# Kernel optimization log

Measured on AMD Instinct MI355X. Metric: run time of the kernel, lower is better.

Reference implementation:

```python
import jax, jax.numpy as jnp
import numpy as np


def _add_self_loops(edge_index, num_nodes):
    loops = jnp.arange(num_nodes, dtype=edge_index.dtype)
    row = jnp.concatenate([edge_index[0], loops])
    col = jnp.concatenate([edge_index[1], loops])
    return row, col


def _gcn_norm(row, col, num_nodes):
    # deg computed at aggregation targets (col), edge weights all 1 (PyG gcn_norm)
    deg = jax.ops.segment_sum(jnp.ones_like(col, dtype=jnp.float32), col,
                              num_segments=num_nodes)
    dinv = jnp.where(deg > 0, jax.lax.rsqrt(deg), 0.0)
    return dinv[row] * dinv[col]  # [E+N]


def _gcn_conv(x, row, col, norm, W, b, num_nodes):
    h = x @ W                                  # [N, out] linear first (PyG GCNConv)
    msg = h[row] * norm[:, None]               # gather + scale, [E+N, out]
    agg = jax.ops.segment_sum(msg, col, num_segments=num_nodes)
    return agg + b


def setup_inputs() -> dict:
    key = jax.random.key(0)
    N, F, H, E = 100000, 128, 64, 1600000
    k1, k2, k3, k4 = jax.random.split(key, 4)
    x = jax.random.normal(k1, (N, F), dtype=jnp.float32)
    edge_index = jax.random.randint(k2, (2, E), 0, N, dtype=jnp.int64)
    s1 = 1.0 / np.sqrt(F)
    s2 = 1.0 / np.sqrt(H)
    W1 = jax.random.normal(k3, (F, H), dtype=jnp.float32) * s1
    b1 = jnp.zeros((H,), dtype=jnp.float32)
    W2 = jax.random.normal(k4, (H, 1), dtype=jnp.float32) * s2
    b2 = jnp.zeros((1,), dtype=jnp.float32)
    return {"x": x, "edge_index": edge_index, "W1": W1, "b1": b1,
            "W2": W2, "b2": b2}


def reference(x, edge_index, W1, b1, W2, b2):
    N = x.shape[0]
    row, col = _add_self_loops(edge_index, N)
    norm = _gcn_norm(row, col, N)
    h = jax.nn.relu(_gcn_conv(x, row, col, norm, W1, b1, N))
    # dropout p=0.0 -> identity
    out = _gcn_conv(h, row, col, norm, W2, b2, N)
    return out.reshape(-1)  # [N]
```

## Files before the change

### kernel.cpp

```cpp
#include <hip/hip_runtime.h>
#include <hip/hip_bf16.h>


#define SHIFT 9
#define BMASK ((1 << SHIFT) - 1)

__device__ __forceinline__ bool detect_i64(const unsigned* u) {
    unsigned acc = 0;
#pragma unroll
    for (int i = 1; i <= 32; ++i) acc |= u[2 * i + 1];
    return acc == 0u;
}

__device__ __forceinline__ int load_edge(const void* ei, bool is64, long long idx) {
    if (is64) return ((const int*)ei)[idx << 1];
    return ((const int*)ei)[idx];
}

__device__ __forceinline__ unsigned bf16_rn(float x) {
    unsigned u = __float_as_uint(x);
    return (u + 0x7fffu + ((u >> 16) & 1u)) >> 16;
}
__device__ __forceinline__ unsigned pack_bf2(float a, float b) {
    return bf16_rn(a) | (bf16_rn(b) << 16);
}
__device__ __forceinline__ float bflo(unsigned v) { return __uint_as_float(v << 16); }
__device__ __forceinline__ float bfhi(unsigned v) {
    return __uint_as_float(v & 0xffff0000u);
}

__global__ __launch_bounds__(256) void binA_kernel(const void* ei, int* gcursor,
                                                   unsigned* __restrict__ pairs, int E,
                                                   int cap) {
    bool is64 = detect_i64((const unsigned*)ei);
    __shared__ int whist[4][256];
    __shared__ int bcur[256];
    int t = threadIdx.x;
    int wid = t >> 6;
    long long per = ((long long)E + gridDim.x - 1) / gridDim.x;
    long long e0 = (long long)blockIdx.x * per;
    long long e1 = e0 + per;
    if (e1 > E) e1 = E;
    whist[0][t] = 0; whist[1][t] = 0; whist[2][t] = 0; whist[3][t] = 0;
    __syncthreads();
    for (long long e = e0 + t; e < e1; e += 256) {
        int c = load_edge(ei, is64, (long long)E + e);
        atomicAdd(&whist[wid][c >> SHIFT], 1);
    }
    __syncthreads();
    int tot = whist[0][t] + whist[1][t] + whist[2][t] + whist[3][t];
    int rel = tot ? atomicAdd(&gcursor[t], tot) : 0;
    bcur[t] = t * cap + rel;
    __syncthreads();
    for (long long e = e0 + t; e < e1; e += 256) {
        int r = load_edge(ei, is64, e);
        int c = load_edge(ei, is64, (long long)E + e);
        int b = c >> SHIFT;
        int rk = atomicAdd(&bcur[b], 1);
        pairs[rk] = ((unsigned)r << SHIFT) | (unsigned)(c & BMASK);
    }
}

__global__ __launch_bounds__(256) void binB_kernel(const unsigned* __restrict__ pairs,
                                                   const int* __restrict__ gcursor,
                                                   int* __restrict__ csr,
                                                   int* __restrict__ offs,
                                                   int* __restrict__ deg, int N,
                                                   int cap) {
    __shared__ int cnt[1 << SHIFT];
    __shared__ int cur[1 << SHIFT];
    __shared__ int tmp[256];
    int b = blockIdx.x, t = threadIdx.x;
    int start = b * cap, end = b * cap + gcursor[b];
    cnt[t] = 0;
    cnt[t + 256] = 0;
    __syncthreads();
    for (int i = start + t; i < end; i += 256) atomicAdd(&cnt[pairs[i] & BMASK], 1);
    __syncthreads();
    int c0 = cnt[2 * t], c1 = cnt[2 * t + 1];
    int s = c0 + c1;
    tmp[t] = s;
    __syncthreads();
    for (int off = 1; off < 256; off <<= 1) {
        int xv = (t >= off) ? tmp[t - off] : 0;
        __syncthreads();
        tmp[t] += xv;
        __syncthreads();
    }
    int excl = tmp[t] - s;
    int p0 = start + excl;
    int p1 = p0 + c0;
    cur[2 * t] = p0;
    cur[2 * t + 1] = p1;
    int node0 = (b << SHIFT) + 2 * t;
    if (node0 < N) { offs[node0] = p0; deg[node0] = c0; }
    if (node0 + 1 < N) { offs[node0 + 1] = p1; deg[node0 + 1] = c1; }
    __syncthreads();
    for (int i = start + t; i < end; i += 256) {
        unsigned p = pairs[i];
        int pos = atomicAdd(&cur[p & BMASK], 1);
        csr[pos] = (int)(p >> SHIFT);
    }
}

__device__ __forceinline__ void fma4(float4& a, float s, const float4& w) {
    a.x = fmaf(s, w.x, a.x);
    a.y = fmaf(s, w.y, a.y);
    a.z = fmaf(s, w.z, a.z);
    a.w = fmaf(s, w.w, a.w);
}

__global__ __launch_bounds__(256) void gemm1_kernel(const float* __restrict__ x,
                                                    const float* __restrict__ W1,
                                                    const int* __restrict__ deg,
                                                    unsigned* __restrict__ hs_u, int N) {
    __shared__ float xs[64][132];
    __shared__ float Wl[128][64];
    int t = threadIdx.x;
    const float4* W4 = (const float4*)W1;
    float4* Wl4 = (float4*)&Wl[0][0];
#pragma unroll
    for (int i = 0; i < 8; ++i) Wl4[t + 256 * i] = W4[t + 256 * i];
    int row0 = blockIdx.x * 64;
    const float4* x4 = (const float4*)x;
#pragma unroll
    for (int i = 0; i < 8; ++i) {
        int idx = t + 256 * i;
        int r = idx >> 5;
        int gr = row0 + r;
        float4 v = (gr < N) ? x4[(long long)gr * 32 + (idx & 31)]
                            : make_float4(0.f, 0.f, 0.f, 0.f);
        *(float4*)&xs[r][(idx & 31) * 4] = v;
    }
    __syncthreads();
    int rg = t >> 4;
    int cg = t & 15;
    float4 acc[4];
#pragma unroll
    for (int i = 0; i < 4; ++i) acc[i] = make_float4(0.f, 0.f, 0.f, 0.f);
#pragma unroll 2
    for (int kk = 0; kk < 128; kk += 4) {
        float4 w0 = *(const float4*)&Wl[kk + 0][cg * 4];
        float4 w1 = *(const float4*)&Wl[kk + 1][cg * 4];
        float4 w2 = *(const float4*)&Wl[kk + 2][cg * 4];
        float4 w3 = *(const float4*)&Wl[kk + 3][cg * 4];
#pragma unroll
        for (int i = 0; i < 4; ++i) {
            float4 xv = *(const float4*)&xs[rg * 4 + i][kk];
            fma4(acc[i], xv.x, w0);
            fma4(acc[i], xv.y, w1);
            fma4(acc[i], xv.z, w2);
            fma4(acc[i], xv.w, w3);
        }
    }
#pragma unroll
    for (int i = 0; i < 4; ++i) {
        int gr = row0 + rg * 4 + i;
        if (gr < N) {
            float dinv = rsqrtf((float)deg[gr] + 1.0f);
            unsigned u0 = pack_bf2(acc[i].x * dinv, acc[i].y * dinv);
            unsigned u1 = pack_bf2(acc[i].z * dinv, acc[i].w * dinv);
            *(uint2*)&hs_u[(size_t)gr * 32 + cg * 2] = make_uint2(u0, u1);
        }
    }
}

#define ACC8(v)                                    \
    a0 += bflo((v).x); a1 += bfhi((v).x);          \
    a2 += bflo((v).y); a3 += bfhi((v).y);          \
    a4 += bflo((v).z); a5 += bfhi((v).z);          \
    a6 += bflo((v).w); a7 += bfhi((v).w);

#define RED8(off)                                  \
    a0 += __shfl_xor(a0, off); a1 += __shfl_xor(a1, off); \
    a2 += __shfl_xor(a2, off); a3 += __shfl_xor(a3, off); \
    a4 += __shfl_xor(a4, off); a5 += __shfl_xor(a5, off); \
    a6 += __shfl_xor(a6, off); a7 += __shfl_xor(a7, off);

__global__ __launch_bounds__(256) void pull1_kernel(
    const uint4* __restrict__ hs4, const int* __restrict__ offs,
    const int* __restrict__ deg, const int* __restrict__ csr,
    const float* __restrict__ b1, const float* __restrict__ W2,
    float* __restrict__ hs2, int N) {
    int gid = blockIdx.x * blockDim.x + threadIdx.x;
    int w = gid >> 6;
    if (w >= N) return;
    int lane = gid & 63;
    int oid = lane >> 3;
    int k = lane & 7;
    int s = offs[w];
    int cnt = deg[w];
    float dinv = rsqrtf((float)cnt + 1.0f);
    float a0 = 0.f, a1 = 0.f, a2 = 0.f, a3 = 0.f;
    float a4 = 0.f, a5 = 0.f, a6 = 0.f, a7 = 0.f;
    if (oid == 0) {
        uint4 v = hs4[(size_t)w * 8 + k];
        ACC8(v);
    }
    for (int base = 0; base < cnt; base += 64) {
        int rem = cnt - base;
        int m = rem < 64 ? rem : 64;
        int r = (lane < m) ? csr[s + base + lane] : 0;
        int tt = 0;
        for (; tt + 32 <= m; tt += 32) {
            int r0 = __shfl(r, tt + oid);
            int r1 = __shfl(r, tt + 8 + oid);
            int r2 = __shfl(r, tt + 16 + oid);
            int r3 = __shfl(r, tt + 24 + oid);
            uint4 v0 = hs4[(size_t)r0 * 8 + k];
            uint4 v1 = hs4[(size_t)r1 * 8 + k];
            uint4 v2 = hs4[(size_t)r2 * 8 + k];
            uint4 v3 = hs4[(size_t)r3 * 8 + k];
            ACC8(v0); ACC8(v1); ACC8(v2); ACC8(v3);
        }
        for (; tt + 8 <= m; tt += 8) {
            int rr = __shfl(r, tt + oid);
            uint4 v = hs4[(size_t)rr * 8 + k];
            ACC8(v);
        }
        if (tt < m) {
            int idx = tt + oid;
            int rr = __shfl(r, idx < m ? idx : 0);
            if (idx < m) {
                uint4 v = hs4[(size_t)rr * 8 + k];
                ACC8(v);
            }
        }
    }
    RED8(8); RED8(16); RED8(32);
    float4 bA = ((const float4*)b1)[2 * k];
    float4 bB = ((const float4*)b1)[2 * k + 1];
    float4 wA = ((const float4*)W2)[2 * k];
    float4 wB = ((const float4*)W2)[2 * k + 1];
    float p = fmaxf(fmaf(dinv, a0, bA.x), 0.f) * wA.x
            + fmaxf(fmaf(dinv, a1, bA.y), 0.f) * wA.y
            + fmaxf(fmaf(dinv, a2, bA.z), 0.f) * wA.z
            + fmaxf(fmaf(dinv, a3, bA.w), 0.f) * wA.w
            + fmaxf(fmaf(dinv, a4, bB.x), 0.f) * wB.x
            + fmaxf(fmaf(dinv, a5, bB.y), 0.f) * wB.y
            + fmaxf(fmaf(dinv, a6, bB.z), 0.f) * wB.z
            + fmaxf(fmaf(dinv, a7, bB.w), 0.f) * wB.w;
    p += __shfl_xor(p, 1);
    p += __shfl_xor(p, 2);
    p += __shfl_xor(p, 4);
    if (lane == 0) hs2[w] = dinv * p;
}

__global__ __launch_bounds__(256) void pull2_kernel(
    const float* __restrict__ hs2, const int* __restrict__ offs,
    const int* __restrict__ deg, const int* __restrict__ csr,
    const float* __restrict__ b2, float* __restrict__ out, int N) {
    int i = blockIdx.x * blockDim.x + threadIdx.x;
    if (i >= N) return;
    int s = offs[i];
    int cnt = deg[i];
    float dinv = rsqrtf((float)cnt + 1.0f);
    float a0 = hs2[i];
    float a1 = 0.f, a2 = 0.f, a3 = 0.f;
    int kk = 0;
    for (; kk + 4 <= cnt; kk += 4) {
        a0 += hs2[csr[s + kk]];
        a1 += hs2[csr[s + kk + 1]];
        a2 += hs2[csr[s + kk + 2]];
        a3 += hs2[csr[s + kk + 3]];
    }
    for (; kk < cnt; ++kk) a0 += hs2[csr[s + kk]];
    out[i] = fmaf(dinv, (a0 + a1) + (a2 + a3), b2[0]);
}

extern "C" void kernel_launch(void* const* d_in, const int* in_sizes, int n_in,
                              void* d_out, int out_size, void* d_ws, size_t ws_size,
                              hipStream_t stream) {
    const float* x = (const float*)d_in[0];
    const void* ei = d_in[1];
    const float* W1 = (const float*)d_in[2];
    const float* b1 = (const float*)d_in[3];
    const float* W2 = (const float*)d_in[4];
    const float* b2 = (const float*)d_in[5];
    float* out = (float*)d_out;

    int N = in_sizes[0] / 128;
    int E = in_sizes[1] / 2;
    int NB = (N + (1 << SHIFT) - 1) >> SHIFT;
    int cap = ((2 * (E / NB)) / 256 + 2) * 256;

    char* p = (char*)d_ws;
    unsigned* hs_u = (unsigned*)p;  p += (size_t)N * 32 * sizeof(unsigned);
    float* hs2 = (float*)p;         p += (size_t)N * sizeof(float);
    int* offs = (int*)p;            p += (size_t)N * sizeof(int);
    int* deg = (int*)p;             p += (size_t)N * sizeof(int);
    unsigned* pairs = (unsigned*)p; p += (size_t)NB * cap * sizeof(unsigned);
    int* csr = (int*)p;             p += (size_t)NB * cap * sizeof(int);
    int* gcursor = (int*)p;         p += 256 * sizeof(int);

    hipMemsetAsync(gcursor, 0, 256 * sizeof(int), stream);
    binA_kernel<<<512, 256, 0, stream>>>(ei, gcursor, pairs, E, cap);
    binB_kernel<<<NB, 256, 0, stream>>>(pairs, gcursor, csr, offs, deg, N, cap);
    gemm1_kernel<<<(N + 63) / 64, 256, 0, stream>>>(x, W1, deg, hs_u, N);
    pull1_kernel<<<((size_t)N * 64 + 255) / 256, 256, 0, stream>>>(
        (const uint4*)hs_u, offs, deg, csr, b1, W2, hs2, N);
    pull2_kernel<<<(N + 255) / 256, 256, 0, stream>>>(hs2, offs, deg, csr, b2, out, N);
}
```

Before: 226.1 us.

## Use split-bf16 MFMA for first GEMM and 8-lane-per-node gather in pull1

The FP32 FMA GEMM in gemm1 is replaced by MFMA 16x16x32 bf16 instructions. Each operand is split into hi and lo bf16 parts, and three products are summed so the result stays close to fp32 accuracy. W1 is stored in LDS with a swizzled layout, and results are staged through LDS so the bf16 rows can be written out coalesced. pull1 now gives each node 8 lanes instead of a full 64-lane wave. Each lane reads CSR indices directly and unrolls 8 neighbor gathers, which removes the shuffles and cross-lane reductions. The trade-off is redundant index loads per lane and possible load imbalance on high-degree nodes.

```diff
diff --git a/kernel.cpp b/kernel.cpp
--- a/kernel.cpp
+++ b/kernel.cpp
@@ -4,6 +4,9 @@
 
 #define SHIFT 9
 #define BMASK ((1 << SHIFT) - 1)
+
+typedef __attribute__((ext_vector_type(8))) short bf16x8;
+typedef __attribute__((ext_vector_type(4))) float f32x4;
 
 __device__ __forceinline__ bool detect_i64(const unsigned* u) {
     unsigned acc = 0;
@@ -103,79 +106,122 @@
     }
 }
 
-__device__ __forceinline__ void fma4(float4& a, float s, const float4& w) {
-    a.x = fmaf(s, w.x, a.x);
-    a.y = fmaf(s, w.y, a.y);
-    a.z = fmaf(s, w.z, a.z);
-    a.w = fmaf(s, w.w, a.w);
-}
-
 __global__ __launch_bounds__(256) void gemm1_kernel(const float* __restrict__ x,
                                                     const float* __restrict__ W1,
                                                     const int* __restrict__ deg,
                                                     unsigned* __restrict__ hs_u, int N) {
-    __shared__ float xs[64][132];
-    __shared__ float Wl[128][64];
+    __shared__ alignas(16) char smem[32768];
+    char* wt_hi = smem;
+    char* wt_lo = smem + 16384;
     int t = threadIdx.x;
-    const float4* W4 = (const float4*)W1;
-    float4* Wl4 = (float4*)&Wl[0][0];
-#pragma unroll
-    for (int i = 0; i < 8; ++i) Wl4[t + 256 * i] = W4[t + 256 * i];
-    int row0 = blockIdx.x * 64;
-    const float4* x4 = (const float4*)x;
-#pragma unroll
-    for (int i = 0; i < 8; ++i) {
+    int l = t & 63;
+    int w = t >> 6;
+
+#pragma unroll
+    for (int i = 0; i < 32; ++i) {
         int idx = t + 256 * i;
-        int r = idx >> 5;
-        int gr = row0 + r;
-        float4 v = (gr < N) ? x4[(long long)gr * 32 + (idx & 31)]
-                            : make_float4(0.f, 0.f, 0.f, 0.f);
-        *(float4*)&xs[r][(idx & 31) * 4] = v;
-    }
-    __syncthreads();
-    int rg = t >> 4;
-    int cg = t & 15;
-    float4 acc[4];
-#pragma unroll
-    for (int i = 0; i < 4; ++i) acc[i] = make_float4(0.f, 0.f, 0.f, 0.f);
-#pragma unroll 2
-    for (int kk = 0; kk < 128; kk += 4) {
-        float4 w0 = *(const float4*)&Wl[kk + 0][cg * 4];
-        float4 w1 = *(const float4*)&Wl[kk + 1][cg * 4];
-        float4 w2 = *(const float4*)&Wl[kk + 2][cg * 4];
-        float4 w3 = *(const float4*)&Wl[kk + 3][cg * 4];
+        int k = idx >> 6;
+        int c = idx & 63;
+        float f = W1[idx];
+        unsigned uh = bf16_rn(f);
+        float fh = __uint_as_float(uh << 16);
+        unsigned ul = bf16_rn(f - fh);
+        int byte = c * 256 + (((k >> 3) ^ (c & 15)) << 4) + ((k & 7) << 1);
+        *(unsigned short*)(wt_hi + byte) = (unsigned short)uh;
+        *(unsigned short*)(wt_lo + byte) = (unsigned short)ul;
+    }
+    __syncthreads();
+
+    int row0 = blockIdx.x * 64 + w * 16;
+    int arow = row0 + (l & 15);
+    bool rok = arow < N;
+    const f32x4* x4 = (const f32x4*)x;
+
+    f32x4 acc[4];
+#pragma unroll
+    for (int ct = 0; ct < 4; ++ct) acc[ct] = (f32x4)(0.f);
+
+#pragma unroll
+    for (int ks = 0; ks < 4; ++ks) {
+        int kbase = ks * 32 + (l >> 4) * 8;
+        f32x4 xa = (f32x4)(0.f), xb = (f32x4)(0.f);
+        if (rok) {
+            xa = x4[(size_t)arow * 32 + (kbase >> 2)];
+            xb = x4[(size_t)arow * 32 + (kbase >> 2) + 1];
+        }
+        unsigned ah[4], al[4];
+#pragma unroll
+        for (int j = 0; j < 4; ++j) {
+            float f0 = (j < 2) ? ((j == 0) ? xa.x : xa.z) : ((j == 2) ? xb.x : xb.z);
+            float f1 = (j < 2) ? ((j == 0) ? xa.y : xa.w) : ((j == 2) ? xb.y : xb.w);
+            unsigned h0 = bf16_rn(f0), h1 = bf16_rn(f1);
+            float r0 = f0 - __uint_as_float(h0 << 16);
+            float r1 = f1 - __uint_as_float(h1 << 16);
+            ah[j] = h0 | (h1 << 16);
+            al[j] = bf16_rn(r0) | (bf16_rn(r1) << 16);
+        }
+        bf16x8 Ah, Al;
+        ((unsigned*)&Ah)[0] = ah[0]; ((unsigned*)&Ah)[1] = ah[1];
+        ((unsigned*)&Ah)[2] = ah[2]; ((unsigned*)&Ah)[3] = ah[3];
+        ((unsigned*)&Al)[0] = al[0]; ((unsigned*)&Al)[1] = al[1];
+        ((unsigned*)&Al)[2] = al[2]; ((unsigned*)&Al)[3] = al[3];
+        int chunk = ks * 4 + (l >> 4);
+#pragma unroll
+        for (int ct = 0; ct < 4; ++ct) {
+            int col = ct * 16 + (l & 15);
+            int byte = col * 256 + ((chunk ^ (col & 15)) << 4);
+            bf16x8 Bh = *(const bf16x8*)(wt_hi + byte);
+            bf16x8 Bl = *(const bf16x8*)(wt_lo + byte);
+            acc[ct] = __builtin_amdgcn_mfma_f32_16x16x32_bf16(Ah, Bh, acc[ct], 0, 0, 0);
+            acc[ct] = __builtin_amdgcn_mfma_f32_16x16x32_bf16(Ah, Bl, acc[ct], 0, 0, 0);
+            acc[ct] = __builtin_amdgcn_mfma_f32_16x16x32_bf16(Al, Bh, acc[ct], 0, 0, 0);
+        }
+    }
+
+    __syncthreads();
+    float* hsb = (float*)(smem) + w * 16 * 68;
+#pragma unroll
+    for (int ct = 0; ct < 4; ++ct) {
 #pragma unroll
         for (int i = 0; i < 4; ++i) {
-            float4 xv = *(const float4*)&xs[rg * 4 + i][kk];
-            fma4(acc[i], xv.x, w0);
-            fma4(acc[i], xv.y, w1);
-            fma4(acc[i], xv.z, w2);
-            fma4(acc[i], xv.w, w3);
+            int row = (l >> 4) * 4 + i;
+            hsb[row * 68 + ct * 16 + (l & 15)] = acc[ct][i];
         }
     }
-#pragma unroll
-    for (int i = 0; i < 4; ++i) {
-        int gr = row0 + rg * 4 + i;
-        if (gr < N) {
-            float dinv = rsqrtf((float)deg[gr] + 1.0f);
-            unsigned u0 = pack_bf2(acc[i].x * dinv, acc[i].y * dinv);
-            unsigned u1 = pack_bf2(acc[i].z * dinv, acc[i].w * dinv);
-            *(uint2*)&hs_u[(size_t)gr * 32 + cg * 2] = make_uint2(u0, u1);
-        }
-    }
-}
-
-#define ACC8(v)                                    \
-    a0 += bflo((v).x); a1 += bfhi((v).x);          \
-    a2 += bflo((v).y); a3 += bfhi((v).y);          \
-    a4 += bflo((v).z); a5 += bfhi((v).z);          \
-    a6 += bflo((v).w); a7 += bfhi((v).w);
-
-#define RED8(off)                                  \
-    a0 += __shfl_xor(a0, off); a1 += __shfl_xor(a1, off); \
-    a2 += __shfl_xor(a2, off); a3 += __shfl_xor(a3, off); \
-    a4 += __shfl_xor(a4, off); a5 += __shfl_xor(a5, off); \
-    a6 += __shfl_xor(a6, off); a7 += __shfl_xor(a7, off);
+    __syncthreads();
+    int row = l & 15;
+    int q = l >> 4;
+    int gr = row0 + row;
+    if (gr < N) {
+        float dinv = rsqrtf((float)deg[gr] + 1.0f);
+        const f32x4* src = (const f32x4*)(hsb + row * 68 + q * 16);
+        f32x4 f0 = src[0], f1 = src[1], f2 = src[2], f3 = src[3];
+        uint4 o0, o1;
+        o0.x = pack_bf2(f0.x * dinv, f0.y * dinv);
+        o0.y = pack_bf2(f0.z * dinv, f0.w * dinv);
+        o0.z = pack_bf2(f1.x * dinv, f1.y * dinv);
+        o0.w = pack_bf2(f1.z * dinv, f1.w * dinv);
+        o1.x = pack_bf2(f2.x * dinv, f2.y * dinv);
+        o1.y = pack_bf2(f2.z * dinv, f2.w * dinv);
+        o1.z = pack_bf2(f3.x * dinv, f3.y * dinv);
+        o1.w = pack_bf2(f3.z * dinv, f3.w * dinv);
+        uint4* dst = (uint4*)&hs_u[(size_t)gr * 32 + q * 8];
+        dst[0] = o0;
+        dst[1] = o1;
+    }
+}
+
+#define ACCV(v)                                            \
+    {                                                      \
+        float2 t0 = make_float2(bflo((v).x), bfhi((v).x)); \
+        float2 t1 = make_float2(bflo((v).y), bfhi((v).y)); \
+        float2 t2 = make_float2(bflo((v).z), bfhi((v).z)); \
+        float2 t3 = make_float2(bflo((v).w), bfhi((v).w)); \
+        a0.x += t0.x; a0.y += t0.y;                        \
+        a1.x += t1.x; a1.y += t1.y;                        \
+        a2.x += t2.x; a2.y += t2.y;                        \
+        a3.x += t3.x; a3.y += t3.y;                        \
+    }
 
 __global__ __launch_bounds__(256) void pull1_kernel(
     const uint4* __restrict__ hs4, const int* __restrict__ offs,
@@ -183,67 +229,60 @@
     const float* __restrict__ b1, const float* __restrict__ W2,
     float* __restrict__ hs2, int N) {
     int gid = blockIdx.x * blockDim.x + threadIdx.x;
-    int w = gid >> 6;
+    int w = gid >> 3;
     if (w >= N) return;
-    int lane = gid & 63;
-    int oid = lane >> 3;
+    int lane = threadIdx.x & 63;
     int k = lane & 7;
     int s = offs[w];
     int cnt = deg[w];
     float dinv = rsqrtf((float)cnt + 1.0f);
-    float a0 = 0.f, a1 = 0.f, a2 = 0.f, a3 = 0.f;
-    float a4 = 0.f, a5 = 0.f, a6 = 0.f, a7 = 0.f;
-    if (oid == 0) {
+    float2 a0 = make_float2(0.f, 0.f), a1 = a0, a2 = a0, a3 = a0;
+    {
         uint4 v = hs4[(size_t)w * 8 + k];
-        ACC8(v);
-    }
-    for (int base = 0; base < cnt; base += 64) {
-        int rem = cnt - base;
-        int m = rem < 64 ? rem : 64;
-        int r = (lane < m) ? csr[s + base + lane] : 0;
-        int tt = 0;
-        for (; tt + 32 <= m; tt += 32) {
-            int r0 = __shfl(r, tt + oid);
-            int r1 = __shfl(r, tt + 8 + oid);
-            int r2 = __shfl(r, tt + 16 + oid);
-            int r3 = __shfl(r, tt + 24 + oid);
-            uint4 v0 = hs4[(size_t)r0 * 8 + k];
-            uint4 v1 = hs4[(size_t)r1 * 8 + k];
-            uint4 v2 = hs4[(size_t)r2 * 8 + k];
-            uint4 v3 = hs4[(size_t)r3 * 8 + k];
-            ACC8(v0); ACC8(v1); ACC8(v2); ACC8(v3);
-        }
-        for (; tt + 8 <= m; tt += 8) {
-            int rr = __shfl(r, tt + oid);
-            uint4 v = hs4[(size_t)rr * 8 + k];
-            ACC8(v);
-        }
-        if (tt < m) {
-            int idx = tt + oid;
-            int rr = __shfl(r, idx < m ? idx : 0);
-            if (idx < m) {
-                uint4 v = hs4[(size_t)rr * 8 + k];
-                ACC8(v);
-            }
-        }
-    }
-    RED8(8); RED8(16); RED8(32);
+        ACCV(v);
+    }
+    int e = 0;
+    for (; e + 8 <= cnt; e += 8) {
+        int r0 = csr[s + e + 0];
+        int r1 = csr[s + e + 1];
+        int r2 = csr[s + e + 2];
+        int r3 = csr[s + e + 3];
+        int r4 = csr[s + e + 4];
+        int r5 = csr[s + e + 5];
+        int r6 = csr[s + e + 6];
+        int r7 = csr[s + e + 7];
+        uint4 v0 = hs4[(size_t)r0 * 8 + k];
+        uint4 v1 = hs4[(size_t)r1 * 8 + k];
+        uint4 v2 = hs4[(size_t)r2 * 8 + k];
+        uint4 v3 = hs4[(size_t)r3 * 8 + k];
+        uint4 v4 = hs4[(size_t)r4 * 8 + k];
+        uint4 v5 = hs4[(size_t)r5 * 8 + k];
+        uint4 v6 = hs4[(size_t)r6 * 8 + k];
+        uint4 v7 = hs4[(size_t)r7 * 8 + k];
+        ACCV(v0); ACCV(v1); ACCV(v2); ACCV(v3);
+        ACCV(v4); ACCV(v5); ACCV(v6); ACCV(v7);
+    }
+    for (; e < cnt; ++e) {
+        int r = csr[s + e];
+        uint4 v = hs4[(size_t)r * 8 + k];
+        ACCV(v);
+    }
     float4 bA = ((const float4*)b1)[2 * k];
     float4 bB = ((const float4*)b1)[2 * k + 1];
     float4 wA = ((const float4*)W2)[2 * k];
     float4 wB = ((const float4*)W2)[2 * k + 1];
-    float p = fmaxf(fmaf(dinv, a0, bA.x), 0.f) * wA.x
-            + fmaxf(fmaf(dinv, a1, bA.y), 0.f) * wA.y
-            + fmaxf(fmaf(dinv, a2, bA.z), 0.f) * wA.z
-            + fmaxf(fmaf(dinv, a3, bA.w), 0.f) * wA.w
-            + fmaxf(fmaf(dinv, a4, bB.x), 0.f) * wB.x
-            + fmaxf(fmaf(dinv, a5, bB.y), 0.f) * wB.y
-            + fmaxf(fmaf(dinv, a6, bB.z), 0.f) * wB.z
-            + fmaxf(fmaf(dinv, a7, bB.w), 0.f) * wB.w;
+    float p = fmaxf(fmaf(dinv, a0.x, bA.x), 0.f) * wA.x
+            + fmaxf(fmaf(dinv, a0.y, bA.y), 0.f) * wA.y
+            + fmaxf(fmaf(dinv, a1.x, bA.z), 0.f) * wA.z
+            + fmaxf(fmaf(dinv, a1.y, bA.w), 0.f) * wA.w
+            + fmaxf(fmaf(dinv, a2.x, bB.x), 0.f) * wB.x
+            + fmaxf(fmaf(dinv, a2.y, bB.y), 0.f) * wB.y
+            + fmaxf(fmaf(dinv, a3.x, bB.z), 0.f) * wB.z
+            + fmaxf(fmaf(dinv, a3.y, bB.w), 0.f) * wB.w;
     p += __shfl_xor(p, 1);
     p += __shfl_xor(p, 2);
     p += __shfl_xor(p, 4);
-    if (lane == 0) hs2[w] = dinv * p;
+    if ((lane & 7) == 0) hs2[w] = dinv * p;
 }
 
 __global__ __launch_bounds__(256) void pull2_kernel(
@@ -293,11 +332,11 @@
     int* csr = (int*)p;             p += (size_t)NB * cap * sizeof(int);
     int* gcursor = (int*)p;         p += 256 * sizeof(int);
 
-    hipMemsetAsync(gcursor, 0, 256 * sizeof(int), stream);
+    (void)hipMemsetAsync(gcursor, 0, 256 * sizeof(int), stream);
     binA_kernel<<<512, 256, 0, stream>>>(ei, gcursor, pairs, E, cap);
     binB_kernel<<<NB, 256, 0, stream>>>(pairs, gcursor, csr, offs, deg, N, cap);
     gemm1_kernel<<<(N + 63) / 64, 256, 0, stream>>>(x, W1, deg, hs_u, N);
-    pull1_kernel<<<((size_t)N * 64 + 255) / 256, 256, 0, stream>>>(
+    pull1_kernel<<<((size_t)N * 8 + 255) / 256, 256, 0, stream>>>(
         (const uint4*)hs_u, offs, deg, csr, b1, W2, hs2, N);
     pull2_kernel<<<(N + 255) / 256, 256, 0, stream>>>(hs2, offs, deg, csr, b2, out, N);
 }
```

Result: faster. 199.0 us (-12.0%).
